# Performance work log

Measured on AMD Instinct MI355X. Metric: run time of the kernel, lower is better.

## Reference

```python
import jax, jax.numpy as jnp
import numpy as np
import math

B, S, D, H = 4, 2048, 1024, 16
HD = D // H
EPS = 1e-10


def setup_inputs() -> dict:
    key = jax.random.key(0)
    kx, kq, kk, kv, ko = jax.random.split(key, 5)
    x = jax.random.normal(kx, (B, S, D), dtype=jnp.float32)
    # causal additive mask: 0 on/below diagonal, -1e9 above
    mask = jnp.where(jnp.triu(jnp.ones((S, S), dtype=bool), k=1), -1e9, 0.0).astype(jnp.float32)
    scale = 1.0 / math.sqrt(D)
    Wq = jax.random.normal(kq, (D, D), dtype=jnp.float32) * scale
    Wk = jax.random.normal(kk, (D, D), dtype=jnp.float32) * scale
    Wv = jax.random.normal(kv, (D, D), dtype=jnp.float32) * scale
    Wo = jax.random.normal(ko, (D, D), dtype=jnp.float32) * scale
    return {"x": x, "mask": mask, "Wq": Wq, "Wk": Wk, "Wv": Wv, "Wo": Wo}


def _nirmalya_softmax(t):
    # faithful to original: plain exp (no max-subtraction), eps in denominator
    p1 = jnp.exp(t)
    return p1 / (jnp.sum(p1, axis=-1, keepdims=True) + EPS)


def reference(x, mask, Wq, Wk, Wv, Wo):
    b, s, d = x.shape
    # torch Linear (bias=False): y = x @ W.T
    def proj(W):
        y = jnp.einsum('bsd,ed->bse', x, W)
        return y.reshape(b, s, H, HD).transpose(0, 2, 1, 3)  # [b,h,s,hd]
    q, k, v = proj(Wq), proj(Wk), proj(Wv)
    scores = jnp.einsum('bhqd,bhkd->bhqk', q, k) / math.sqrt(HD)
    scores = scores + mask  # broadcast over batch/heads
    attn = _nirmalya_softmax(scores)
    out = jnp.einsum('bhqk,bhkd->bhqd', attn, v)
    out = out.transpose(0, 2, 1, 3).reshape(b, s, d)
    return jnp.einsum('bsd,ed->bse', out, Wo)
```

## Files before the change

### kernel.cpp

```cpp
#include <hip/hip_runtime.h>
#include <hip/hip_bf16.h>

typedef __bf16 bf16;
typedef __attribute__((ext_vector_type(8))) __bf16 bf16x8;
typedef __attribute__((ext_vector_type(4))) float f32x4;
typedef __attribute__((ext_vector_type(16))) float f32x16;
typedef __attribute__((ext_vector_type(2))) unsigned int u32x2;
typedef __attribute__((ext_vector_type(4))) unsigned int u32x4;

#define MFMA16(a, b, c) __builtin_amdgcn_mfma_f32_16x16x32_bf16((a), (b), (c), 0, 0, 0)
#define MFMA32(a, b, c) __builtin_amdgcn_mfma_f32_32x32x16_bf16((a), (b), (c), 0, 0, 0)

#define GLOAD_LDS16(gp, lp)                                                              \
  __builtin_amdgcn_global_load_lds(                                                      \
      (const __attribute__((address_space(1))) unsigned int*)(gp),                       \
      (__attribute__((address_space(3))) unsigned int*)(lp), 16, 0, 0)

#define BAR()   __builtin_amdgcn_s_barrier()
#define LGKM0() asm volatile("s_waitcnt lgkmcnt(0)" ::: "memory")
#define VMC(n)  asm volatile("s_waitcnt vmcnt(" #n ")" ::: "memory")
#define PRIO1() __builtin_amdgcn_s_setprio(1)
#define PRIO0() __builtin_amdgcn_s_setprio(0)

__global__ __launch_bounds__(256) void cvt_all(const float* __restrict__ x,
                                               const float* __restrict__ wq,
                                               const float* __restrict__ wk,
                                               const float* __restrict__ wv,
                                               const float* __restrict__ wo,
                                               bf16* __restrict__ xb,
                                               bf16* __restrict__ wqkv,
                                               bf16* __restrict__ wob) {
  constexpr int NXC = 8388608 / 8;
  constexpr int NWC = 1048576 / 8;
  constexpr int TOT = NXC + 4 * NWC;
  for (int c = blockIdx.x * 256 + threadIdx.x; c < TOT; c += gridDim.x * 256) {
    const float* src; bf16* dst; int idx;
    if (c < NXC) { src = x; dst = xb; idx = c; }
    else {
      int c2 = c - NXC; int wsel = c2 >> 17; idx = c2 & (NWC - 1);
      src = wsel == 0 ? wq : wsel == 1 ? wk : wsel == 2 ? wv : wo;
      dst = wsel < 3 ? wqkv + (size_t)wsel * 1048576 : wob;
    }
    float4 v0 = reinterpret_cast<const float4*>(src)[idx * 2];
    float4 v1 = reinterpret_cast<const float4*>(src)[idx * 2 + 1];
    bf16x8 o;
    o[0] = (bf16)v0.x; o[1] = (bf16)v0.y; o[2] = (bf16)v0.z; o[3] = (bf16)v0.w;
    o[4] = (bf16)v1.x; o[5] = (bf16)v1.y; o[6] = (bf16)v1.z; o[7] = (bf16)v1.w;
    reinterpret_cast<bf16x8*>(dst)[idx] = o;
  }
}

#define MMA8(BF, MH, NH)                                                                 \
  _Pragma("unroll") for (int mi = 0; mi < 2; ++mi)                                       \
  _Pragma("unroll") for (int ni = 0; ni < 2; ++ni)                                       \
  _Pragma("unroll") for (int ks = 0; ks < 2; ++ks)                                       \
      acc[(MH) * 2 + mi][(NH) * 2 + ni] =                                                \
          MFMA16(af[mi][ks], (BF)[ni][ks], acc[(MH) * 2 + mi][(NH) * 2 + ni]);

template <int MODE, int NT>
__global__ __launch_bounds__(512, 1) void gemm8(const bf16* __restrict__ A,
                                                const bf16* __restrict__ B,
                                                void* __restrict__ Cv,
                                                bf16* __restrict__ VT) {
  constexpr int K = 1024;
  __shared__ bf16 smem[49152];
  const int tid = threadIdx.x, lane = tid & 63, w = tid >> 6;
  const int l15 = lane & 15, l16 = lane >> 4;
  const int wr = w >> 2, wc = w & 3;
  const int lin = blockIdx.x;
  const int idx = lin >> 3;
  const int mt = (lin & 7) * 8 + idx / NT;
  const int nt = idx % NT;
  const int bm0 = mt * 128, bn0 = nt * 256;

  auto stA = [&](int buf, int t, int j) {
    const int r = j * 64 + (tid >> 3);
    const int g = (tid & 7) ^ (r & 7);
    GLOAD_LDS16(&A[(size_t)(bm0 + r) * K + t * 64 + g * 8],
                &smem[buf * 8192 + j * 4096 + tid * 8]);
  };
  auto stB = [&](int buf, int t, int j) {
    const int r = j * 64 + (tid >> 3);
    const int g = (tid & 7) ^ (r & 7);
    GLOAD_LDS16(&B[(size_t)(bn0 + r) * K + t * 64 + g * 8],
                &smem[16384 + buf * 16384 + j * 4096 + tid * 8]);
  };
  bf16x8 af[2][2], b0[2][2], b1[2][2];
  auto ldA = [&](int buf, int mh, bf16x8 (&dst)[2][2]) {
#pragma unroll
    for (int mi = 0; mi < 2; ++mi)
#pragma unroll
      for (int ks = 0; ks < 2; ++ks)
        dst[mi][ks] = *reinterpret_cast<const bf16x8*>(
            &smem[buf * 8192 + (wr * 64 + mh * 32 + mi * 16 + l15) * 64 +
                  (((ks * 4 + l16) ^ (l15 & 7)) * 8)]);
  };
  auto ldB = [&](int buf, int nh, bf16x8 (&dst)[2][2]) {
#pragma unroll
    for (int ni = 0; ni < 2; ++ni)
#pragma unroll
      for (int ks = 0; ks < 2; ++ks)
        dst[ni][ks] = *reinterpret_cast<const bf16x8*>(
            &smem[16384 + buf * 16384 + (wc * 64 + nh * 32 + ni * 16 + l15) * 64 +
                  (((ks * 4 + l16) ^ (l15 & 7)) * 8)]);
  };

  f32x4 acc[4][4] = {};

  stA(0, 0, 0); stA(0, 0, 1);
  stB(0, 0, 0); stB(0, 0, 1); stB(0, 0, 2); stB(0, 0, 3);
  stA(1, 1, 0); stA(1, 1, 1);
  stB(1, 1, 0); stB(1, 1, 1); stB(1, 1, 2); stB(1, 1, 3);
  VMC(6); BAR();

#pragma unroll 1
  for (int it = 0; it < K / 128; ++it) {
    const int t0 = 2 * it;
    const bool last = (it == K / 128 - 1);
    ldA(0, 0, af); ldB(0, 0, b0);
    BAR(); LGKM0();
    PRIO1(); MMA8(b0, 0, 0); PRIO0();
    BAR();
    ldB(0, 1, b1);
    BAR(); LGKM0();
    PRIO1(); MMA8(b1, 0, 1); PRIO0();
    BAR();
    ldA(0, 1, af);
    BAR(); LGKM0();
    PRIO1(); MMA8(b1, 1, 1); PRIO0();
    BAR();
    if (!last) {
      stA(0, t0 + 2, 0); stA(0, t0 + 2, 1);
      stB(0, t0 + 2, 0); stB(0, t0 + 2, 1); stB(0, t0 + 2, 2); stB(0, t0 + 2, 3);
    }
    PRIO1(); MMA8(b0, 1, 0); PRIO0();
    if (last) { VMC(0); } else { VMC(6); }
    BAR();
    ldA(1, 0, af); ldB(1, 0, b0);
    BAR(); LGKM0();
    PRIO1(); MMA8(b0, 0, 0); PRIO0();
    BAR();
    ldB(1, 1, b1);
    BAR(); LGKM0();
    PRIO1(); MMA8(b1, 0, 1); PRIO0();
    BAR();
    ldA(1, 1, af);
    BAR(); LGKM0();
    PRIO1(); MMA8(b1, 1, 1); PRIO0();
    BAR();
    if (!last) {
      stA(1, t0 + 3, 0); stA(1, t0 + 3, 1);
      stB(1, t0 + 3, 0); stB(1, t0 + 3, 1); stB(1, t0 + 3, 2); stB(1, t0 + 3, 3);
    }
    PRIO1(); MMA8(b0, 1, 0); PRIO0();
    if (!last) VMC(6);
    BAR();
  }

  if constexpr (MODE == 0) {
#pragma unroll
    for (int i = 0; i < 4; ++i)
#pragma unroll
      for (int j = 0; j < 4; ++j)
#pragma unroll
        for (int r = 0; r < 4; ++r) {
          const size_t row = bm0 + wr * 64 + (i >> 1) * 32 + (i & 1) * 16 + l16 * 4 + r;
          const size_t col = bn0 + wc * 64 + (j >> 1) * 32 + (j & 1) * 16 + l15;
          reinterpret_cast<float*>(Cv)[row * (NT * 256) + col] = acc[i][j][r];
        }
  } else {
    if (bn0 < 2048) {
#pragma unroll
      for (int i = 0; i < 4; ++i)
#pragma unroll
        for (int j = 0; j < 4; ++j)
#pragma unroll
          for (int r = 0; r < 4; ++r) {
            const size_t row = bm0 + wr * 64 + (i >> 1) * 32 + (i & 1) * 16 + l16 * 4 + r;
            const size_t col = bn0 + wc * 64 + (j >> 1) * 32 + (j & 1) * 16 + l15;
            float v = acc[i][j][r];
            if (col < 1024) v *= 0.18033688011112042f;
            reinterpret_cast<bf16*>(Cv)[row * 2048 + col] = (bf16)v;
          }
    } else {
#pragma unroll
      for (int i = 0; i < 4; ++i)
#pragma unroll
        for (int j = 0; j < 4; ++j)
#pragma unroll
          for (int r = 0; r < 4; ++r) {
            const int m = wr * 64 + (i >> 1) * 32 + (i & 1) * 16 + l16 * 4 + r;
            const int n = wc * 64 + (j >> 1) * 32 + (j & 1) * 16 + l15;
            smem[n * 136 + m] = (bf16)acc[i][j][r];
          }
      BAR();
      const int n = tid >> 1, half = tid & 1;
      const size_t vbase = ((size_t)(bm0 >> 11) * 1024 + (bn0 - 2048 + n)) * 2048 +
                           (bm0 & 2047) + half * 64;
#pragma unroll
      for (int k = 0; k < 8; ++k) {
        bf16x8 v = *reinterpret_cast<const bf16x8*>(&smem[n * 136 + half * 64 + k * 8]);
        *reinterpret_cast<bf16x8*>(&VT[vbase + k * 8]) = v;
      }
    }
  }
}

constexpr int S_ = 2048, H_ = 16, LDQK = 2048;

__global__ __launch_bounds__(128, 2) void attn_kernel(const bf16* __restrict__ QK,
                                                      const bf16* __restrict__ VT,
                                                      bf16* __restrict__ AO) {
  __shared__ bf16 Ks[2][64 * 64];
  __shared__ bf16 Vs[2][64 * 64];
  const int tid = threadIdx.x, lane = tid & 63, w = tid >> 6;
  const int l31 = lane & 31, hi = lane >> 5;
  const int x7 = l31 & 7;
  const int bh = blockIdx.x, b = bh >> 4, h = bh & (H_ - 1);
  const int pairid = blockIdx.y;
  const size_t qoff = (size_t)b * S_ * LDQK + h * 64;
  const size_t koff = qoff + 1024;
  const size_t voff = (size_t)bh * 64 * LDQK;
  const size_t aoff = (size_t)b * S_ * 1024 + h * 64;

  auto stK = [&](int t) {
    const int kv0 = t * 64, bs = t & 1;
#pragma unroll
    for (int i = 0; i < 4; ++i) {
      const int c = tid + 128 * i;
      const int row = c >> 3, gs = (c & 7) ^ (row & 7);
      GLOAD_LDS16(&QK[koff + (size_t)(kv0 + row) * LDQK + gs * 8], &Ks[bs][c * 8]);
    }
  };
  auto stV = [&](int t) {
    const int kv0 = t * 64, bs = t & 1;
#pragma unroll
    for (int i = 0; i < 4; ++i) {
      const int c = tid + 128 * i;
      const int row = c >> 3, gs = (c & 7) ^ (row & 7);
      GLOAD_LDS16(&VT[voff + (size_t)row * LDQK + kv0 + gs * 8], &Vs[bs][c * 8]);
    }
  };

#pragma unroll 1
  for (int half = 0; half < 2; ++half) {
    const int j = half ? (31 - pairid) : pairid;
    const int qbase = j * 64 + w * 32;
    const int ntiles = j + 1;
    const int qg = qbase + l31;

    bf16x8 qf[4];
#pragma unroll
    for (int ks = 0; ks < 4; ++ks)
      qf[ks] = *reinterpret_cast<const bf16x8*>(
          &QK[qoff + (size_t)qg * LDQK + ks * 16 + hi * 8]);

    f32x16 oT[2] = {};
    float rs = 0.0f;
    f32x16 scA[2], scB[2];

    auto qkt = [&](int t, f32x16 (&sc)[2]) {
      const int bs = t & 1;
      f32x16 zz = {};
      sc[0] = zz; sc[1] = zz;
      PRIO1();
#pragma unroll
      for (int ks = 0; ks < 4; ++ks) {
        bf16x8 kf0 = *reinterpret_cast<bf16x8*>(
            &Ks[bs][l31 * 64 + (((ks * 2 + hi) ^ x7) * 8)]);
        bf16x8 kf1 = *reinterpret_cast<bf16x8*>(
            &Ks[bs][(32 + l31) * 64 + (((ks * 2 + hi) ^ x7) * 8)]);
        sc[0] = MFMA32(kf0, qf[ks], sc[0]);
        sc[1] = MFMA32(kf1, qf[ks], sc[1]);
      }
      PRIO0();
    };

    auto softpv = [&](int t, f32x16 (&sc)[2]) {
      const bool diag = (t == j);
      const int kv0 = t * 64;
      const int hi4 = hi * 4;
#pragma unroll
      for (int hh = 0; hh < 2; ++hh)
#pragma unroll
        for (int r = 0; r < 16; ++r) {
          float e;
          asm("v_exp_f32 %0, %1" : "=v"(e) : "v"(sc[hh][r]));
          if (diag) {
            const int kvg = kv0 + hh * 32 + (r & 3) + 8 * (r >> 2) + hi4;
            e = (kvg <= qg) ? e : 0.0f;
          }
          rs += e;
          sc[hh][r] = e;
        }
      u32x4 pf[4];
#pragma unroll
      for (int hh = 0; hh < 2; ++hh)
#pragma unroll
        for (int q4 = 0; q4 < 2; ++q4) {
          unsigned x0, x1, y0, y1;
          asm("v_cvt_pk_bf16_f32 %0, %1, %2" : "=v"(x0)
              : "v"(sc[hh][q4 * 8 + 0]), "v"(sc[hh][q4 * 8 + 1]));
          asm("v_cvt_pk_bf16_f32 %0, %1, %2" : "=v"(x1)
              : "v"(sc[hh][q4 * 8 + 2]), "v"(sc[hh][q4 * 8 + 3]));
          asm("v_cvt_pk_bf16_f32 %0, %1, %2" : "=v"(y0)
              : "v"(sc[hh][q4 * 8 + 4]), "v"(sc[hh][q4 * 8 + 5]));
          asm("v_cvt_pk_bf16_f32 %0, %1, %2" : "=v"(y1)
              : "v"(sc[hh][q4 * 8 + 6]), "v"(sc[hh][q4 * 8 + 7]));
          asm("v_permlane32_swap_b32 %0, %1" : "+v"(x0), "+v"(y0));
          asm("v_permlane32_swap_b32 %0, %1" : "+v"(x1), "+v"(y1));
          pf[hh * 2 + q4][0] = x0; pf[hh * 2 + q4][1] = x1;
          pf[hh * 2 + q4][2] = y0; pf[hh * 2 + q4][3] = y1;
        }
      const int bs = t & 1;
      PRIO1();
#pragma unroll
      for (int ks = 0; ks < 4; ++ks) {
        bf16x8 vt0 = *reinterpret_cast<bf16x8*>(
            &Vs[bs][l31 * 64 + (((ks * 2 + hi) ^ x7) * 8)]);
        bf16x8 vt1 = *reinterpret_cast<bf16x8*>(
            &Vs[bs][(32 + l31) * 64 + (((ks * 2 + hi) ^ x7) * 8)]);
        oT[0] = MFMA32(vt0, *reinterpret_cast<bf16x8*>(&pf[ks]), oT[0]);
        oT[1] = MFMA32(vt1, *reinterpret_cast<bf16x8*>(&pf[ks]), oT[1]);
      }
      PRIO0();
    };

    auto step = [&](int t, f32x16 (&cur)[2], f32x16 (&nxt)[2]) {
      if (t + 2 < ntiles) stK(t + 2);
      if (t + 1 < ntiles) { stV(t + 1); qkt(t + 1, nxt); }
      softpv(t, cur);
      VMC(0); BAR();
    };

    stK(0); stV(0);
    if (ntiles > 1) stK(1);
    VMC(0); BAR();
    qkt(0, scA);
    BAR();

#pragma unroll 1
    for (int t = 0; t < ntiles; t += 2) {
      step(t, scA, scB);
      if (t + 1 < ntiles) step(t + 1, scB, scA);
    }

    const float rst = rs + __shfl_xor(rs, 32);
    const float inv = 1.0f / (rst + 1e-10f);

    bf16* lo = &Ks[0][0] + w * 2048;
#pragma unroll
    for (int dh = 0; dh < 2; ++dh)
#pragma unroll
      for (int rq = 0; rq < 4; ++rq) {
        const float v0 = oT[dh][rq * 4 + 0] * inv, v1 = oT[dh][rq * 4 + 1] * inv;
        const float v2 = oT[dh][rq * 4 + 2] * inv, v3 = oT[dh][rq * 4 + 3] * inv;
        unsigned d0, d1;
        asm("v_cvt_pk_bf16_f32 %0, %1, %2" : "=v"(d0) : "v"(v0), "v"(v1));
        asm("v_cvt_pk_bf16_f32 %0, %1, %2" : "=v"(d1) : "v"(v2), "v"(v3));
        u32x2 dd; dd[0] = d0; dd[1] = d1;
        *reinterpret_cast<u32x2*>(
            &lo[l31 * 64 + (((dh * 4 + rq) ^ x7) * 8) + hi * 4]) = dd;
      }
#pragma unroll
    for (int jj = 0; jj < 4; ++jj) {
      const int gran = lane + 64 * jj;
      const int qr = gran >> 3, g = gran & 7;
      bf16x8 vv = *reinterpret_cast<bf16x8*>(&lo[qr * 64 + ((g ^ (qr & 7)) * 8)]);
      *reinterpret_cast<bf16x8*>(
          &AO[aoff + (size_t)(j * 64 + w * 32 + qr) * 1024 + g * 8]) = vv;
    }
    LGKM0(); BAR();
  }
}

extern "C" void kernel_launch(void* const* d_in, const int* in_sizes, int n_in,
                              void* d_out, int out_size, void* d_ws, size_t ws_size,
                              hipStream_t stream) {
  const float* x  = (const float*)d_in[0];
  const float* Wq = (const float*)d_in[2];
  const float* Wk = (const float*)d_in[3];
  const float* Wv = (const float*)d_in[4];
  const float* Wo = (const float*)d_in[5];

  constexpr int B = 4, S = 2048, D = 1024;
  constexpr size_t nx = (size_t)B * S * D;
  constexpr size_t nw = (size_t)D * D;

  char* ws = (char*)d_ws;
  bf16* xb    = (bf16*)ws;
  bf16* Wqkvb = xb + nx;
  bf16* Wob   = Wqkvb + 3 * nw;
  bf16* QKb   = Wob + nw;
  bf16* VTb   = QKb + (size_t)B * S * 2048;
  bf16* AOb   = VTb + nx;

  cvt_all<<<2048, 256, 0, stream>>>(x, Wq, Wk, Wv, Wo, xb, Wqkvb, Wob);

  gemm8<2, 12><<<768, 512, 0, stream>>>(xb, Wqkvb, QKb, VTb);

  attn_kernel<<<dim3(B * H_, 16), 128, 0, stream>>>(QKb, VTb, AOb);

  gemm8<0, 4><<<256, 512, 0, stream>>>(AOb, Wob, d_out, nullptr);
}
```

Measured before the change: 159.8 us.

## Rework GEMM tiles to 256-row blocks with simplified two-phase pipeline

Replaces the 128x256 GEMM kernel with a templated version that uses 256-row A tiles and a configurable N width: 256 for the QKV projection and 128 for the output projection. Each warp now holds a 128xN accumulator and the inner loop runs fewer barriered phases, with B fragments loaded once per k-step. The aim is more data reuse per tile and less barrier overhead. The QKV projection now launches 384 blocks, which is fewer than the GPU's CU count of about 256 times two waves and gives uneven waves. Register pressure is also higher. The V-transpose epilogue is split into two halves so it fits in LDS.

```diff
diff --git a/kernel.cpp b/kernel.cpp
--- a/kernel.cpp
+++ b/kernel.cpp
@@ -50,157 +50,149 @@
   }
 }
 
-#define MMA8(BF, MH, NH)                                                                 \
-  _Pragma("unroll") for (int mi = 0; mi < 2; ++mi)                                       \
-  _Pragma("unroll") for (int ni = 0; ni < 2; ++ni)                                       \
+#define MMAH(MH)                                                                         \
+  _Pragma("unroll") for (int mi = 0; mi < 4; ++mi)                                       \
+  _Pragma("unroll") for (int ni = 0; ni < NFRAG; ++ni)                                   \
   _Pragma("unroll") for (int ks = 0; ks < 2; ++ks)                                       \
-      acc[(MH) * 2 + mi][(NH) * 2 + ni] =                                                \
-          MFMA16(af[mi][ks], (BF)[ni][ks], acc[(MH) * 2 + mi][(NH) * 2 + ni]);
-
-template <int MODE, int NT>
-__global__ __launch_bounds__(512, 1) void gemm8(const bf16* __restrict__ A,
-                                                const bf16* __restrict__ B,
-                                                void* __restrict__ Cv,
-                                                bf16* __restrict__ VT) {
+      acc[(MH) * 4 + mi][ni] = MFMA16(af[mi][ks], bfr[ni][ks], acc[(MH) * 4 + mi][ni]);
+
+template <int MODE, int NT, int NFRAG>
+__global__ __launch_bounds__(512, 1) void gemm2p(const bf16* __restrict__ A,
+                                                 const bf16* __restrict__ B,
+                                                 void* __restrict__ Cv,
+                                                 bf16* __restrict__ VT) {
   constexpr int K = 1024;
-  __shared__ bf16 smem[49152];
+  constexpr int BN = NFRAG * 64;
+  constexpr int BSZ = BN * 64;
+  __shared__ bf16 smem[32768 + 2 * BSZ];
   const int tid = threadIdx.x, lane = tid & 63, w = tid >> 6;
   const int l15 = lane & 15, l16 = lane >> 4;
   const int wr = w >> 2, wc = w & 3;
   const int lin = blockIdx.x;
   const int idx = lin >> 3;
-  const int mt = (lin & 7) * 8 + idx / NT;
+  const int mt = (lin & 7) * 4 + idx / NT;
   const int nt = idx % NT;
-  const int bm0 = mt * 128, bn0 = nt * 256;
-
-  auto stA = [&](int buf, int t, int j) {
-    const int r = j * 64 + (tid >> 3);
-    const int g = (tid & 7) ^ (r & 7);
-    GLOAD_LDS16(&A[(size_t)(bm0 + r) * K + t * 64 + g * 8],
-                &smem[buf * 8192 + j * 4096 + tid * 8]);
-  };
-  auto stB = [&](int buf, int t, int j) {
-    const int r = j * 64 + (tid >> 3);
-    const int g = (tid & 7) ^ (r & 7);
-    GLOAD_LDS16(&B[(size_t)(bn0 + r) * K + t * 64 + g * 8],
-                &smem[16384 + buf * 16384 + j * 4096 + tid * 8]);
-  };
-  bf16x8 af[2][2], b0[2][2], b1[2][2];
-  auto ldA = [&](int buf, int mh, bf16x8 (&dst)[2][2]) {
-#pragma unroll
-    for (int mi = 0; mi < 2; ++mi)
+  const int bm0 = mt * 256, bn0 = nt * BN;
+
+  auto stage = [&](int t, int buf) {
+#pragma unroll
+    for (int j = 0; j < 4; ++j) {
+      const int r = j * 64 + (tid >> 3);
+      const int g = (tid & 7) ^ (r & 7);
+      GLOAD_LDS16(&A[(size_t)(bm0 + r) * K + t * 64 + g * 8],
+                  &smem[buf * 16384 + j * 4096 + tid * 8]);
+    }
+#pragma unroll
+    for (int j = 0; j < NFRAG; ++j) {
+      const int r = j * 64 + (tid >> 3);
+      const int g = (tid & 7) ^ (r & 7);
+      GLOAD_LDS16(&B[(size_t)(bn0 + r) * K + t * 64 + g * 8],
+                  &smem[32768 + buf * BSZ + j * 4096 + tid * 8]);
+    }
+  };
+
+  bf16x8 af[4][2], bfr[NFRAG][2];
+  auto ldA = [&](int buf, int mh) {
+#pragma unroll
+    for (int mi = 0; mi < 4; ++mi)
 #pragma unroll
       for (int ks = 0; ks < 2; ++ks)
-        dst[mi][ks] = *reinterpret_cast<const bf16x8*>(
-            &smem[buf * 8192 + (wr * 64 + mh * 32 + mi * 16 + l15) * 64 +
+        af[mi][ks] = *reinterpret_cast<const bf16x8*>(
+            &smem[buf * 16384 + (wr * 128 + mh * 64 + mi * 16 + l15) * 64 +
                   (((ks * 4 + l16) ^ (l15 & 7)) * 8)]);
   };
-  auto ldB = [&](int buf, int nh, bf16x8 (&dst)[2][2]) {
-#pragma unroll
-    for (int ni = 0; ni < 2; ++ni)
+  auto ldB = [&](int buf) {
+#pragma unroll
+    for (int ni = 0; ni < NFRAG; ++ni)
 #pragma unroll
       for (int ks = 0; ks < 2; ++ks)
-        dst[ni][ks] = *reinterpret_cast<const bf16x8*>(
-            &smem[16384 + buf * 16384 + (wc * 64 + nh * 32 + ni * 16 + l15) * 64 +
+        bfr[ni][ks] = *reinterpret_cast<const bf16x8*>(
+            &smem[32768 + buf * BSZ + (wc * (NFRAG * 16) + ni * 16 + l15) * 64 +
                   (((ks * 4 + l16) ^ (l15 & 7)) * 8)]);
   };
 
-  f32x4 acc[4][4] = {};
-
-  stA(0, 0, 0); stA(0, 0, 1);
-  stB(0, 0, 0); stB(0, 0, 1); stB(0, 0, 2); stB(0, 0, 3);
-  stA(1, 1, 0); stA(1, 1, 1);
-  stB(1, 1, 0); stB(1, 1, 1); stB(1, 1, 2); stB(1, 1, 3);
-  VMC(6); BAR();
+  f32x4 acc[8][NFRAG] = {};
+
+  stage(0, 0); stage(1, 1);
+  if constexpr (NFRAG == 4) { VMC(8); } else { VMC(6); }
+  BAR();
 
 #pragma unroll 1
   for (int it = 0; it < K / 128; ++it) {
     const int t0 = 2 * it;
     const bool last = (it == K / 128 - 1);
-    ldA(0, 0, af); ldB(0, 0, b0);
-    BAR(); LGKM0();
-    PRIO1(); MMA8(b0, 0, 0); PRIO0();
-    BAR();
-    ldB(0, 1, b1);
-    BAR(); LGKM0();
-    PRIO1(); MMA8(b1, 0, 1); PRIO0();
-    BAR();
-    ldA(0, 1, af);
-    BAR(); LGKM0();
-    PRIO1(); MMA8(b1, 1, 1); PRIO0();
+    ldB(0); ldA(0, 0);
+    LGKM0(); PRIO1(); MMAH(0); PRIO0();
+    ldA(0, 1);
+    LGKM0(); PRIO1(); MMAH(1); PRIO0();
+    BAR();
+    if (!last) stage(t0 + 2, 0);
+    if (last) { VMC(0); }
+    else if constexpr (NFRAG == 4) { VMC(8); } else { VMC(6); }
+    BAR();
+    ldB(1); ldA(1, 0);
+    LGKM0(); PRIO1(); MMAH(0); PRIO0();
+    ldA(1, 1);
+    LGKM0(); PRIO1(); MMAH(1); PRIO0();
     BAR();
     if (!last) {
-      stA(0, t0 + 2, 0); stA(0, t0 + 2, 1);
-      stB(0, t0 + 2, 0); stB(0, t0 + 2, 1); stB(0, t0 + 2, 2); stB(0, t0 + 2, 3);
-    }
-    PRIO1(); MMA8(b0, 1, 0); PRIO0();
-    if (last) { VMC(0); } else { VMC(6); }
-    BAR();
-    ldA(1, 0, af); ldB(1, 0, b0);
-    BAR(); LGKM0();
-    PRIO1(); MMA8(b0, 0, 0); PRIO0();
-    BAR();
-    ldB(1, 1, b1);
-    BAR(); LGKM0();
-    PRIO1(); MMA8(b1, 0, 1); PRIO0();
-    BAR();
-    ldA(1, 1, af);
-    BAR(); LGKM0();
-    PRIO1(); MMA8(b1, 1, 1); PRIO0();
-    BAR();
-    if (!last) {
-      stA(1, t0 + 3, 0); stA(1, t0 + 3, 1);
-      stB(1, t0 + 3, 0); stB(1, t0 + 3, 1); stB(1, t0 + 3, 2); stB(1, t0 + 3, 3);
-    }
-    PRIO1(); MMA8(b0, 1, 0); PRIO0();
-    if (!last) VMC(6);
+      stage(t0 + 3, 1);
+      if constexpr (NFRAG == 4) { VMC(8); } else { VMC(6); }
+    }
     BAR();
   }
 
   if constexpr (MODE == 0) {
-#pragma unroll
-    for (int i = 0; i < 4; ++i)
-#pragma unroll
-      for (int j = 0; j < 4; ++j)
-#pragma unroll
-        for (int r = 0; r < 4; ++r) {
-          const size_t row = bm0 + wr * 64 + (i >> 1) * 32 + (i & 1) * 16 + l16 * 4 + r;
-          const size_t col = bn0 + wc * 64 + (j >> 1) * 32 + (j & 1) * 16 + l15;
-          reinterpret_cast<float*>(Cv)[row * (NT * 256) + col] = acc[i][j][r];
+    constexpr int NC = NT * BN;
+#pragma unroll
+    for (int i = 0; i < 8; ++i)
+#pragma unroll
+      for (int ni = 0; ni < NFRAG; ++ni)
+#pragma unroll
+        for (int rr = 0; rr < 4; ++rr) {
+          const size_t row = bm0 + wr * 128 + (i >> 2) * 64 + (i & 3) * 16 + l16 * 4 + rr;
+          const size_t col = bn0 + wc * (NFRAG * 16) + ni * 16 + l15;
+          reinterpret_cast<float*>(Cv)[row * NC + col] = acc[i][ni][rr];
         }
   } else {
     if (bn0 < 2048) {
 #pragma unroll
-      for (int i = 0; i < 4; ++i)
-#pragma unroll
-        for (int j = 0; j < 4; ++j)
-#pragma unroll
-          for (int r = 0; r < 4; ++r) {
-            const size_t row = bm0 + wr * 64 + (i >> 1) * 32 + (i & 1) * 16 + l16 * 4 + r;
-            const size_t col = bn0 + wc * 64 + (j >> 1) * 32 + (j & 1) * 16 + l15;
-            float v = acc[i][j][r];
+      for (int i = 0; i < 8; ++i)
+#pragma unroll
+        for (int ni = 0; ni < 4; ++ni)
+#pragma unroll
+          for (int rr = 0; rr < 4; ++rr) {
+            const size_t row = bm0 + wr * 128 + (i >> 2) * 64 + (i & 3) * 16 + l16 * 4 + rr;
+            const size_t col = bn0 + wc * 64 + ni * 16 + l15;
+            float v = acc[i][ni][rr];
             if (col < 1024) v *= 0.18033688011112042f;
             reinterpret_cast<bf16*>(Cv)[row * 2048 + col] = (bf16)v;
           }
     } else {
-#pragma unroll
-      for (int i = 0; i < 4; ++i)
-#pragma unroll
-        for (int j = 0; j < 4; ++j)
-#pragma unroll
-          for (int r = 0; r < 4; ++r) {
-            const int m = wr * 64 + (i >> 1) * 32 + (i & 1) * 16 + l16 * 4 + r;
-            const int n = wc * 64 + (j >> 1) * 32 + (j & 1) * 16 + l15;
-            smem[n * 136 + m] = (bf16)acc[i][j][r];
-          }
-      BAR();
-      const int n = tid >> 1, half = tid & 1;
-      const size_t vbase = ((size_t)(bm0 >> 11) * 1024 + (bn0 - 2048 + n)) * 2048 +
-                           (bm0 & 2047) + half * 64;
-#pragma unroll
-      for (int k = 0; k < 8; ++k) {
-        bf16x8 v = *reinterpret_cast<const bf16x8*>(&smem[n * 136 + half * 64 + k * 8]);
-        *reinterpret_cast<bf16x8*>(&VT[vbase + k * 8]) = v;
+#pragma unroll 1
+      for (int hh = 0; hh < 2; ++hh) {
+        if (wr == hh) {
+#pragma unroll
+          for (int i = 0; i < 8; ++i)
+#pragma unroll
+            for (int ni = 0; ni < 4; ++ni)
+#pragma unroll
+              for (int rr = 0; rr < 4; ++rr) {
+                const int ml = (i >> 2) * 64 + (i & 3) * 16 + l16 * 4 + rr;
+                const int nl = wc * 64 + ni * 16 + l15;
+                smem[nl * 136 + ml] = (bf16)acc[i][ni][rr];
+              }
+        }
+        BAR();
+        const int n = tid >> 1, mseg = tid & 1;
+        const size_t vb = ((size_t)(bm0 >> 11) * 1024 + (bn0 - 2048 + n)) * 2048 +
+                          (bm0 & 2047) + hh * 128 + mseg * 64;
+#pragma unroll
+        for (int k = 0; k < 8; ++k) {
+          bf16x8 v = *reinterpret_cast<const bf16x8*>(&smem[n * 136 + mseg * 64 + k * 8]);
+          *reinterpret_cast<bf16x8*>(&VT[vb + k * 8]) = v;
+        }
+        BAR();
       }
     }
   }
@@ -397,9 +389,9 @@
 
   cvt_all<<<2048, 256, 0, stream>>>(x, Wq, Wk, Wv, Wo, xb, Wqkvb, Wob);
 
-  gemm8<2, 12><<<768, 512, 0, stream>>>(xb, Wqkvb, QKb, VTb);
+  gemm2p<2, 12, 4><<<384, 512, 0, stream>>>(xb, Wqkvb, QKb, VTb);
 
   attn_kernel<<<dim3(B * H_, 16), 128, 0, stream>>>(QKb, VTb, AOb);
 
-  gemm8<0, 4><<<256, 512, 0, stream>>>(AOb, Wob, d_out, nullptr);
+  gemm2p<0, 8, 2><<<256, 512, 0, stream>>>(AOb, Wob, d_out, nullptr);
 }
```

New measurement: 166.9 us. +4.4%, slower.

## Use 256x256 block tile for QKV projection GEMM

Applied to the files above, without the earlier changes.

Replaces the templated 128x256-tile QKV GEMM with a dedicated 256x256-tile kernel using 128KB LDS double buffering. Each wave now computes 128x64 outputs, with interleaved half-tile loads and a two-phase transposed V write-out through shared memory. The larger tile is meant to halve the operand reloads from global/L2 per output and raise MFMA density. In exchange it launches only 384 blocks (about 1.5 waves on 256 CUs), which risks tail imbalance, and it adds register pressure. The output GEMM is split out into its own non-templated fp32 kernel.

```diff
diff --git a/kernel.cpp b/kernel.cpp
--- a/kernel.cpp
+++ b/kernel.cpp
@@ -50,6 +50,162 @@
   }
 }
 
+#define MMAQ(BF, MH, NH)                                                                 \
+  _Pragma("unroll") for (int mi = 0; mi < 4; ++mi)                                       \
+  _Pragma("unroll") for (int ni = 0; ni < 2; ++ni)                                       \
+  _Pragma("unroll") for (int ks = 0; ks < 2; ++ks)                                       \
+      acc[(MH) * 4 + mi][(NH) * 2 + ni] =                                                \
+          MFMA16(af[mi][ks], (BF)[ni][ks], acc[(MH) * 4 + mi][(NH) * 2 + ni]);
+
+__global__ __launch_bounds__(512, 1) void gemm256_qkv(const bf16* __restrict__ A,
+                                                      const bf16* __restrict__ B,
+                                                      bf16* __restrict__ QK,
+                                                      bf16* __restrict__ VT) {
+  constexpr int K = 1024;
+  __shared__ bf16 smem[65536];
+  bf16* Asm = smem;
+  bf16* Bsm = smem + 32768;
+  const int tid = threadIdx.x, lane = tid & 63, w = tid >> 6;
+  const int l15 = lane & 15, l16 = lane >> 4;
+  const int wr = w >> 2, wc = w & 3;
+  const int lin = blockIdx.x;
+  const int idx = lin >> 3;
+  const int mt = (lin & 7) * 4 + idx / 12;
+  const int nt = idx % 12;
+  const int bm0 = mt * 256, bn0 = nt * 256;
+
+  auto stA = [&](int buf, int t, int h) {
+#pragma unroll
+    for (int i = 0; i < 2; ++i) {
+      const int c = tid + 512 * i, rh = c >> 3;
+      const int r = (rh & 63) | (h << 6) | ((rh >> 6) << 7);
+      const int g = (c & 7) ^ (r & 7);
+      GLOAD_LDS16(&A[(size_t)(bm0 + r) * K + t * 64 + g * 8],
+                  &Asm[buf * 16384 + r * 64 + (c & 7) * 8]);
+    }
+  };
+  auto stB = [&](int buf, int t, int h) {
+#pragma unroll
+    for (int i = 0; i < 2; ++i) {
+      const int c = tid + 512 * i, rh = c >> 3;
+      const int r = (rh & 31) | (h << 5) | ((rh >> 5) << 6);
+      const int g = (c & 7) ^ (r & 7);
+      GLOAD_LDS16(&B[(size_t)(bn0 + r) * K + t * 64 + g * 8],
+                  &Bsm[buf * 16384 + r * 64 + (c & 7) * 8]);
+    }
+  };
+  bf16x8 af[4][2], b0[2][2], b1[2][2];
+  auto ldA = [&](int buf, int mh) {
+#pragma unroll
+    for (int mi = 0; mi < 4; ++mi)
+#pragma unroll
+      for (int ks = 0; ks < 2; ++ks)
+        af[mi][ks] = *reinterpret_cast<const bf16x8*>(
+            &Asm[buf * 16384 + (wr * 128 + mh * 64 + mi * 16 + l15) * 64 +
+                 (((ks * 4 + l16) ^ (l15 & 7)) * 8)]);
+  };
+  auto ldB = [&](int buf, int nh, bf16x8 (&dst)[2][2]) {
+#pragma unroll
+    for (int ni = 0; ni < 2; ++ni)
+#pragma unroll
+      for (int ks = 0; ks < 2; ++ks)
+        dst[ni][ks] = *reinterpret_cast<const bf16x8*>(
+            &Bsm[buf * 16384 + (wc * 64 + nh * 32 + ni * 16 + l15) * 64 +
+                 (((ks * 4 + l16) ^ (l15 & 7)) * 8)]);
+  };
+
+  f32x4 acc[8][4] = {};
+
+  stA(0, 0, 0); stB(0, 0, 0); stB(0, 0, 1); stA(0, 0, 1);
+  stA(1, 1, 0); stB(1, 1, 0); stB(1, 1, 1);
+  VMC(6); BAR();
+
+#pragma unroll 1
+  for (int it = 0; it < K / 128; ++it) {
+    const int t0 = 2 * it;
+    const bool last = (it == K / 128 - 1);
+    ldA(0, 0); ldB(0, 0, b0);
+    stA(1, t0 + 1, 1);
+    BAR(); LGKM0();
+    PRIO1(); MMAQ(b0, 0, 0); PRIO0();
+    BAR();
+    ldB(0, 1, b1);
+    if (!last) stA(0, t0 + 2, 0);
+    BAR(); LGKM0();
+    PRIO1(); MMAQ(b1, 0, 1); PRIO0();
+    BAR();
+    ldA(0, 1);
+    if (!last) stB(0, t0 + 2, 0);
+    BAR(); LGKM0();
+    PRIO1(); MMAQ(b1, 1, 1); PRIO0();
+    BAR();
+    if (!last) stB(0, t0 + 2, 1);
+    PRIO1(); MMAQ(b0, 1, 0); PRIO0();
+    if (last) { VMC(0); } else { VMC(6); }
+    BAR();
+    ldA(1, 0); ldB(1, 0, b0);
+    if (!last) stA(0, t0 + 2, 1);
+    BAR(); LGKM0();
+    PRIO1(); MMAQ(b0, 0, 0); PRIO0();
+    BAR();
+    ldB(1, 1, b1);
+    if (!last) stA(1, t0 + 3, 0);
+    BAR(); LGKM0();
+    PRIO1(); MMAQ(b1, 0, 1); PRIO0();
+    BAR();
+    ldA(1, 1);
+    if (!last) stB(1, t0 + 3, 0);
+    BAR(); LGKM0();
+    PRIO1(); MMAQ(b1, 1, 1); PRIO0();
+    BAR();
+    if (!last) stB(1, t0 + 3, 1);
+    PRIO1(); MMAQ(b0, 1, 0); PRIO0();
+    if (!last) VMC(6);
+    BAR();
+  }
+
+  if (bn0 < 2048) {
+#pragma unroll
+    for (int i = 0; i < 8; ++i)
+#pragma unroll
+      for (int ni = 0; ni < 4; ++ni)
+#pragma unroll
+        for (int rr = 0; rr < 4; ++rr) {
+          const size_t row = bm0 + wr * 128 + i * 16 + l16 * 4 + rr;
+          const size_t col = bn0 + wc * 64 + ni * 16 + l15;
+          float v = acc[i][ni][rr];
+          if (col < 1024) v *= 0.18033688011112042f;
+          QK[row * 2048 + col] = (bf16)v;
+        }
+  } else {
+#pragma unroll 1
+    for (int hh = 0; hh < 2; ++hh) {
+      if (wr == hh) {
+#pragma unroll
+        for (int i = 0; i < 8; ++i)
+#pragma unroll
+          for (int ni = 0; ni < 4; ++ni)
+#pragma unroll
+            for (int rr = 0; rr < 4; ++rr) {
+              const int ml = i * 16 + l16 * 4 + rr;
+              const int nl = wc * 64 + ni * 16 + l15;
+              smem[nl * 136 + ml] = (bf16)acc[i][ni][rr];
+            }
+      }
+      BAR();
+      const int n = tid >> 1, mseg = tid & 1;
+      const size_t vb = ((size_t)(bm0 >> 11) * 1024 + (bn0 - 2048 + n)) * 2048 +
+                        (bm0 & 2047) + hh * 128 + mseg * 64;
+#pragma unroll
+      for (int k = 0; k < 8; ++k) {
+        bf16x8 v = *reinterpret_cast<const bf16x8*>(&smem[n * 136 + mseg * 64 + k * 8]);
+        *reinterpret_cast<bf16x8*>(&VT[vb + k * 8]) = v;
+      }
+      BAR();
+    }
+  }
+}
+
 #define MMA8(BF, MH, NH)                                                                 \
   _Pragma("unroll") for (int mi = 0; mi < 2; ++mi)                                       \
   _Pragma("unroll") for (int ni = 0; ni < 2; ++ni)                                       \
@@ -57,12 +213,10 @@
       acc[(MH) * 2 + mi][(NH) * 2 + ni] =                                                \
           MFMA16(af[mi][ks], (BF)[ni][ks], acc[(MH) * 2 + mi][(NH) * 2 + ni]);
 
-template <int MODE, int NT>
-__global__ __launch_bounds__(512, 1) void gemm8(const bf16* __restrict__ A,
-                                                const bf16* __restrict__ B,
-                                                void* __restrict__ Cv,
-                                                bf16* __restrict__ VT) {
-  constexpr int K = 1024;
+__global__ __launch_bounds__(512, 1) void gemm8_f32(const bf16* __restrict__ A,
+                                                    const bf16* __restrict__ B,
+                                                    float* __restrict__ C) {
+  constexpr int K = 1024, NT = 4;
   __shared__ bf16 smem[49152];
   const int tid = threadIdx.x, lane = tid & 63, w = tid >> 6;
   const int l15 = lane & 15, l16 = lane >> 4;
@@ -157,53 +311,16 @@
     BAR();
   }
 
-  if constexpr (MODE == 0) {
-#pragma unroll
-    for (int i = 0; i < 4; ++i)
-#pragma unroll
-      for (int j = 0; j < 4; ++j)
-#pragma unroll
-        for (int r = 0; r < 4; ++r) {
-          const size_t row = bm0 + wr * 64 + (i >> 1) * 32 + (i & 1) * 16 + l16 * 4 + r;
-          const size_t col = bn0 + wc * 64 + (j >> 1) * 32 + (j & 1) * 16 + l15;
-          reinterpret_cast<float*>(Cv)[row * (NT * 256) + col] = acc[i][j][r];
-        }
-  } else {
-    if (bn0 < 2048) {
-#pragma unroll
-      for (int i = 0; i < 4; ++i)
-#pragma unroll
-        for (int j = 0; j < 4; ++j)
-#pragma unroll
-          for (int r = 0; r < 4; ++r) {
-            const size_t row = bm0 + wr * 64 + (i >> 1) * 32 + (i & 1) * 16 + l16 * 4 + r;
-            const size_t col = bn0 + wc * 64 + (j >> 1) * 32 + (j & 1) * 16 + l15;
-            float v = acc[i][j][r];
-            if (col < 1024) v *= 0.18033688011112042f;
-            reinterpret_cast<bf16*>(Cv)[row * 2048 + col] = (bf16)v;
-          }
-    } else {
-#pragma unroll
-      for (int i = 0; i < 4; ++i)
-#pragma unroll
-        for (int j = 0; j < 4; ++j)
-#pragma unroll
-          for (int r = 0; r < 4; ++r) {
-            const int m = wr * 64 + (i >> 1) * 32 + (i & 1) * 16 + l16 * 4 + r;
-            const int n = wc * 64 + (j >> 1) * 32 + (j & 1) * 16 + l15;
-            smem[n * 136 + m] = (bf16)acc[i][j][r];
-          }
-      BAR();
-      const int n = tid >> 1, half = tid & 1;
-      const size_t vbase = ((size_t)(bm0 >> 11) * 1024 + (bn0 - 2048 + n)) * 2048 +
-                           (bm0 & 2047) + half * 64;
-#pragma unroll
-      for (int k = 0; k < 8; ++k) {
-        bf16x8 v = *reinterpret_cast<const bf16x8*>(&smem[n * 136 + half * 64 + k * 8]);
-        *reinterpret_cast<bf16x8*>(&VT[vbase + k * 8]) = v;
+#pragma unroll
+  for (int i = 0; i < 4; ++i)
+#pragma unroll
+    for (int j = 0; j < 4; ++j)
+#pragma unroll
+      for (int r = 0; r < 4; ++r) {
+        const size_t row = bm0 + wr * 64 + (i >> 1) * 32 + (i & 1) * 16 + l16 * 4 + r;
+        const size_t col = bn0 + wc * 64 + (j >> 1) * 32 + (j & 1) * 16 + l15;
+        C[row * 1024 + col] = acc[i][j][r];
       }
-    }
-  }
 }
 
 constexpr int S_ = 2048, H_ = 16, LDQK = 2048;
@@ -397,9 +514,9 @@
 
   cvt_all<<<2048, 256, 0, stream>>>(x, Wq, Wk, Wv, Wo, xb, Wqkvb, Wob);
 
-  gemm8<2, 12><<<768, 512, 0, stream>>>(xb, Wqkvb, QKb, VTb);
+  gemm256_qkv<<<384, 512, 0, stream>>>(xb, Wqkvb, QKb, VTb);
 
   attn_kernel<<<dim3(B * H_, 16), 128, 0, stream>>>(QKb, VTb, AOb);
 
-  gemm8<0, 4><<<256, 512, 0, stream>>>(AOb, Wob, d_out, nullptr);
+  gemm8_f32<<<256, 512, 0, stream>>>(AOb, Wob, (float*)d_out);
 }
```

New measurement: 163.3 us. 1.02x slower.
